# Performance work log

Measured on AMD Instinct MI355X. Metric: run time of the kernel, lower is better.

Reference implementation:

```python
import jax, jax.numpy as jnp
import numpy as np

D_MODEL = 1024
HIDDEN = 2048          # config.max_neurons
MOE_DIM = 64           # hardcoded moe_hidden_dim
N_EXPERTS = 8
TOP_K = 2
EXP_HIDDEN = HIDDEN // 2  # 1024
B, S = 4, 2048


def setup_inputs() -> dict:
    key = jax.random.key(0)
    ks = jax.random.split(key, 20)
    def w(k, shape, fan_in):
        return (jax.random.normal(k, shape, dtype=jnp.float32) / np.sqrt(fan_in)).astype(jnp.float32)
    return {
        "inputs_embeds": jax.random.normal(ks[0], (B, S, D_MODEL), dtype=jnp.float32),
        # GIFNeuron encoder (d_model -> hidden)
        "enc_w": w(ks[1], (D_MODEL, HIDDEN), D_MODEL),
        "enc_b": jnp.zeros((HIDDEN,), jnp.float32),
        # SpikeToContinuousBridge (hidden -> moe_dim)
        "s2c_w": w(ks[2], (HIDDEN, MOE_DIM), HIDDEN),
        "s2c_b": jnp.zeros((MOE_DIM,), jnp.float32),
        # LiquidMoERouter MLP (moe_dim -> 64 -> n_experts)
        "r_w1": w(ks[3], (MOE_DIM, 64), MOE_DIM),
        "r_b1": jnp.zeros((64,), jnp.float32),
        "r_w2": w(ks[4], (64, N_EXPERTS), 64),
        "r_b2": jnp.zeros((N_EXPERTS,), jnp.float32),
        # SNNExpert stacks (moe_dim -> exp_hidden -> moe_dim)
        "e_w1": w(ks[5], (N_EXPERTS, MOE_DIM, EXP_HIDDEN), MOE_DIM),
        "e_b1": jnp.zeros((N_EXPERTS, EXP_HIDDEN), jnp.float32),
        "e_w2": w(ks[6], (N_EXPERTS, EXP_HIDDEN, MOE_DIM), EXP_HIDDEN),
        "e_b2": jnp.zeros((N_EXPERTS, MOE_DIM), jnp.float32),
        # ContinuousToSpikeBridge (moe_dim -> hidden), poisson rates
        "c2s_w": w(ks[7], (MOE_DIM, HIDDEN), MOE_DIM),
        "c2s_b": jnp.zeros((HIDDEN,), jnp.float32),
        # GIFNeuron decoder (hidden -> d_model)
        "dec_w": w(ks[8], (HIDDEN, D_MODEL), HIDDEN),
        "dec_b": jnp.zeros((D_MODEL,), jnp.float32),
        # output LayerNorm
        "ln_g": jnp.ones((D_MODEL,), jnp.float32),
        "ln_b": jnp.zeros((D_MODEL,), jnp.float32),
    }


def reference(inputs_embeds, enc_w, enc_b, s2c_w, s2c_b, r_w1, r_b1, r_w2, r_b2,
              e_w1, e_b1, e_w2, e_b2, c2s_w, c2s_b, dec_w, dec_b, ln_g, ln_b):
    b, s, _ = inputs_embeds.shape
    # encoder GIF neuron: linear + sigmoid surrogate spikes -> [B,S,H]
    spikes = jax.nn.sigmoid(inputs_embeds @ enc_w + enc_b)
    # rate-decode (time axis of length 1 is identity) + projection -> [N, MOE_DIM]
    cont = spikes.reshape(b * s, -1) @ s2c_w + s2c_b
    # router: MLP -> softmax -> top-2 (renormalized)
    rh = jax.nn.relu(cont @ r_w1 + r_b1)
    probs = jax.nn.softmax(rh @ r_w2 + r_b2, axis=-1)          # [N, E]
    topw, topi = jax.lax.top_k(probs, TOP_K)                    # [N, K]
    topw = topw / jnp.sum(topw, axis=-1, keepdims=True)
    # combine weights per token per expert: sum_k w_k * [idx_k == e]
    comb = jnp.sum(jax.nn.one_hot(topi, N_EXPERTS, dtype=cont.dtype) * topw[..., None], axis=1)  # [N, E]
    # dense grouped expert compute (equivalent to masked gather/scatter loop)
    eh = jax.nn.relu(jnp.einsum('nd,edh->neh', cont, e_w1) + e_b1)   # [N, E, EXP_HIDDEN]
    eo = jnp.einsum('neh,ehd->ned', eh, e_w2) + e_b2                  # [N, E, MOE_DIM]
    moe_out = jnp.einsum('ned,ne->nd', eo, comb)                      # [N, MOE_DIM]
    # poisson-rate encode to spike space; mean over L identical rate steps == rates
    rates = jax.nn.sigmoid(moe_out @ c2s_w + c2s_b)                   # [N, H]
    x = rates.reshape(b, s, -1)
    # decoder GIF neuron + LayerNorm
    dec = jax.nn.sigmoid(x @ dec_w + dec_b)                           # [B, S, D]
    mu = jnp.mean(dec, axis=-1, keepdims=True)
    var = jnp.var(dec, axis=-1, keepdims=True)
    return (dec - mu) * jax.lax.rsqrt(var + 1e-5) * ln_g + ln_b
```

## Files before the change

kernel.cpp:

```cpp
#include <hip/hip_runtime.h>
#include <hip/hip_bf16.h>
#include <math.h>

typedef float  f32x4  __attribute__((ext_vector_type(4)));
typedef __bf16 bf16x8 __attribute__((ext_vector_type(8)));

__device__ __forceinline__ unsigned short f2bf(float f){
  union { float f; unsigned u; } v; v.f = f;
  unsigned u = v.u;
  return (unsigned short)((u + 0x7FFFu + ((u >> 16) & 1u)) >> 16);
}
__device__ __forceinline__ float bf2f(unsigned short h){
  union { unsigned u; float f; } v; v.u = ((unsigned)h) << 16;
  return v.f;
}
__device__ __forceinline__ void gload_lds16(const void* g, void* l){
  __builtin_amdgcn_global_load_lds((__attribute__((address_space(1))) void*)g,
                                   (__attribute__((address_space(3))) void*)l, 16, 0, 0);
}
__device__ __forceinline__ float sigmoidf_(float x){ return 1.f / (1.f + expf(-x)); }

__global__ __launch_bounds__(256)
void split_x_kernel(const float* __restrict__ X, unsigned short* __restrict__ A){
  for (int i = blockIdx.x*256 + threadIdx.x; i < 8192*1024; i += gridDim.x*256){
    int row = i >> 10, col = i & 1023;
    float x = X[i];
    unsigned short h = f2bf(x);
    unsigned short l = f2bf(x - bf2f(h));
    unsigned short* Ar = A + (size_t)row*3072 + col;
    Ar[0]    = h;
    Ar[1024] = l;
    Ar[2048] = h;
  }
}

__global__ __launch_bounds__(256)
void prep_tiles(const float* __restrict__ enc_w, const float* __restrict__ dec_w,
                const float* __restrict__ e_w1, const float* __restrict__ e_w2,
                const float* __restrict__ c2s_w,
                unsigned short* __restrict__ BtE, unsigned short* __restrict__ decT,
                unsigned short* __restrict__ W1T, unsigned short* __restrict__ W2T,
                unsigned short* __restrict__ c2sT)
{
  __shared__ unsigned tile[64*65];
  const int t = threadIdx.x;
  const int b = blockIdx.x;

  const float* src; long sbase; int sld, r0, c0;
  if (b < 512)        { src = enc_w; sbase = 0;                    sld = 2048; r0 = (b>>5)*64;       c0 = (b&31)*64; }
  else if (b < 1024)  { int q=b-512;  src = dec_w; sbase = 0;      sld = 1024; r0 = (q>>4)*64;       c0 = (q&15)*64; }
  else if (b < 1152)  { int q=b-1024; src = e_w1;  sbase = (long)(q>>4)*65536; sld = 1024; r0 = 0;   c0 = (q&15)*64; }
  else if (b < 1280)  { int q=b-1152; src = e_w2;  sbase = (long)(q>>4)*65536; sld = 64;   r0 = (q&15)*64; c0 = 0; }
  else                { int q=b-1280; src = c2s_w; sbase = 0;      sld = 2048; r0 = 0;              c0 = q*64; }

  #pragma unroll
  for (int it = 0; it < 4; ++it){
    int r  = it*16 + (t>>4);
    int c4 = (t&15)*4;
    float4 v = *(const float4*)&src[sbase + (long)(r0+r)*sld + c0 + c4];
    float vv[4] = {v.x, v.y, v.z, v.w};
    #pragma unroll
    for (int e = 0; e < 4; ++e){
      unsigned short h = f2bf(vv[e]);
      unsigned short l = f2bf(vv[e] - bf2f(h));
      tile[(c4+e)*65 + r] = (unsigned)h | ((unsigned)l << 16);
    }
  }
  __syncthreads();

  #pragma unroll
  for (int it = 0; it < 2; ++it){
    int c  = it*32 + (t>>3);
    int kc = (t&7)*8;
    unsigned short hi8[8], lo8[8];
    #pragma unroll
    for (int e = 0; e < 8; ++e){
      unsigned p = tile[c*65 + kc + e];
      hi8[e] = (unsigned short)(p & 0xFFFFu);
      lo8[e] = (unsigned short)(p >> 16);
    }
    if (b < 512){
      unsigned short* dst = BtE + (size_t)(c0 + c)*3072 + r0 + kc;
      *(uint4*)(dst)        = *(const uint4*)hi8;
      *(uint4*)(dst + 1024) = *(const uint4*)hi8;
      *(uint4*)(dst + 2048) = *(const uint4*)lo8;
    } else if (b < 1024){
      *(uint4*)(decT + (size_t)(c0 + c)*2048 + r0 + kc) = *(const uint4*)hi8;
    } else if (b < 1152){
      int e = (b-1024) >> 4;
      *(uint4*)(W1T + ((size_t)e<<16) + (size_t)(c0 + c)*64 + kc) = *(const uint4*)hi8;
    } else if (b < 1280){
      int e = (b-1152) >> 4;
      *(uint4*)(W2T + ((size_t)e<<16) + (size_t)(c0 + c)*1024 + r0 + kc) = *(const uint4*)hi8;
    } else {
      *(uint4*)(c2sT + (size_t)(c0 + c)*64 + kc) = *(const uint4*)hi8;
    }
  }
}

template<int SIG, int OBF>
__global__ __launch_bounds__(256)
void gemm_bt(const unsigned short* __restrict__ A, const unsigned short* __restrict__ Bt,
             const float* __restrict__ bias, void* __restrict__ C,
             int M, int N, int K)
{
  __shared__ alignas(16) unsigned short As[128*64];
  __shared__ alignas(16) unsigned short Bs[128*64];
  const int t = threadIdx.x;
  const int wid = t >> 6, lane = t & 63;
  const int nbn = N >> 7;
  const int q = gridDim.x >> 3;
  const int bid = (int)blockIdx.x;
  const int sb = (bid & 7) * q + (bid >> 3);
  const int bm = sb / nbn, bn = sb % nbn;
  const int wm = wid >> 1, wn = wid & 1;

  f32x4 acc[4][4];
  #pragma unroll
  for (int i=0;i<4;++i)
    #pragma unroll
    for (int j=0;j<4;++j) acc[i][j] = (f32x4){0.f,0.f,0.f,0.f};

  const size_t Kb = (size_t)K * 2;
  const char* Ab = (const char*)A  + (size_t)(bm*128) * Kb;
  const char* Bb = (const char*)Bt + (size_t)(bn*128) * Kb;

  for (int k0 = 0; k0 < K; k0 += 64){
    #pragma unroll
    for (int i = 0; i < 4; ++i){
      int L  = ((i*4 + wid) << 10) + (lane << 4);
      int r  = L >> 7;
      int cb = L & 127;
      int sb2 = cb ^ ((r & 7) << 4);
      gload_lds16(Ab + (size_t)r*Kb + (size_t)k0*2 + sb2, (char*)As + ((i*4+wid)<<10));
      gload_lds16(Bb + (size_t)r*Kb + (size_t)k0*2 + sb2, (char*)Bs + ((i*4+wid)<<10));
    }
    __syncthreads();
    #pragma unroll
    for (int ks = 0; ks < 64; ks += 32){
      bf16x8 af[4], bg[4];
      const int cb = ks*2 + ((lane >> 4) << 4);
      #pragma unroll
      for (int i = 0; i < 4; ++i){
        int ra = wm*64 + i*16 + (lane & 15);
        af[i] = *(const bf16x8*)((const char*)As + (ra<<7) + (cb ^ ((ra&7)<<4)));
        int rb = wn*64 + i*16 + (lane & 15);
        bg[i] = *(const bf16x8*)((const char*)Bs + (rb<<7) + (cb ^ ((rb&7)<<4)));
      }
      #pragma unroll
      for (int i = 0; i < 4; ++i)
        #pragma unroll
        for (int j = 0; j < 4; ++j)
          acc[i][j] = __builtin_amdgcn_mfma_f32_16x16x32_bf16(af[i], bg[j], acc[i][j], 0, 0, 0);
    }
    __syncthreads();
  }

  const int mrow0 = bm*128 + wm*64;
  const int ncol0 = bn*128 + wn*64;
  #pragma unroll
  for (int i = 0; i < 4; ++i){
    int row = mrow0 + i*16 + ((lane>>4)<<2);
    #pragma unroll
    for (int j = 0; j < 4; ++j){
      int col = ncol0 + j*16 + (lane & 15);
      float bv = bias[col];
      #pragma unroll
      for (int r = 0; r < 4; ++r){
        float v = acc[i][j][r] + bv;
        if (SIG) v = sigmoidf_(v);
        if (OBF) ((unsigned short*)C)[(size_t)(row + r)*N + col] = f2bf(v);
        else     ((float*)C)[(size_t)(row + r)*N + col] = v;
      }
    }
  }
}

__global__ __launch_bounds__(256)
void s2c_split(const float* __restrict__ spikes, const float* __restrict__ w,
               float* __restrict__ part)
{
  __shared__ float wS[4][64*64];
  const int t = threadIdx.x, wid = t >> 6, lane = t & 63;
  const int tg = blockIdx.x >> 2;
  const int ck = ((blockIdx.x & 3) << 2) | wid;
  const int tok = tg*64 + lane;
  const int k0 = ck * 128;

  float acc[64];
  #pragma unroll
  for (int j=0;j<64;++j) acc[j] = 0.f;

  const float* srow = spikes + (size_t)tok*2048 + k0;
  float* wsp = wS[wid];

  for (int half = 0; half < 2; ++half){
    const float* gsrc = w + (size_t)(k0 + half*64)*64;
    #pragma unroll
    for (int it = 0; it < 16; ++it){
      int idx = (it*64 + lane)*4;
      *(float4*)&wsp[idx] = *(const float4*)&gsrc[idx];
    }
    #pragma unroll 2
    for (int kq = 0; kq < 16; ++kq){
      float4 s4 = *(const float4*)&srow[half*64 + kq*4];
      const float sv[4] = {s4.x, s4.y, s4.z, s4.w};
      #pragma unroll
      for (int ki = 0; ki < 4; ++ki){
        const float* wrow = &wsp[(kq*4+ki)*64];
        #pragma unroll
        for (int j4 = 0; j4 < 16; ++j4){
          float4 wv = *(const float4*)&wrow[j4*4];
          acc[j4*4+0] += sv[ki] * wv.x;
          acc[j4*4+1] += sv[ki] * wv.y;
          acc[j4*4+2] += sv[ki] * wv.z;
          acc[j4*4+3] += sv[ki] * wv.w;
        }
      }
    }
  }
  float* po = part + ((size_t)ck*8192 + tok)*64;
  #pragma unroll
  for (int j4 = 0; j4 < 16; ++j4){
    float4 o; o.x = acc[j4*4+0]; o.y = acc[j4*4+1]; o.z = acc[j4*4+2]; o.w = acc[j4*4+3];
    *(float4*)&po[j4*4] = o;
  }
}

__global__ __launch_bounds__(256)
void s2c_reduce(const float* __restrict__ part, const float* __restrict__ bias,
                float* __restrict__ cont, unsigned short* __restrict__ contbf)
{
  int i4 = blockIdx.x*256 + threadIdx.x;
  int base = i4 * 4;
  float4 a = {0.f,0.f,0.f,0.f};
  #pragma unroll
  for (int c = 0; c < 16; ++c){
    float4 p = *(const float4*)&part[(size_t)c*524288 + base];
    a.x += p.x; a.y += p.y; a.z += p.z; a.w += p.w;
  }
  int j0 = base & 63;
  float4 b = *(const float4*)&bias[j0];
  a.x += b.x; a.y += b.y; a.z += b.z; a.w += b.w;
  *(float4*)&cont[base] = a;
  unsigned short h0 = f2bf(a.x), h1 = f2bf(a.y), h2 = f2bf(a.z), h3 = f2bf(a.w);
  unsigned u0 = ((unsigned)h1 << 16) | h0;
  unsigned u1 = ((unsigned)h3 << 16) | h2;
  uint2 u; u.x = u0; u.y = u1;
  *(uint2*)&contbf[base] = u;
}

__global__ __launch_bounds__(256)
void router_kernel(const float* __restrict__ cont, const float* __restrict__ w1,
                   const float* __restrict__ b1, const float* __restrict__ w2,
                   const float* __restrict__ b2, float* __restrict__ comb)
{
  __shared__ float w1s[64*64];
  __shared__ float w2s[64*8];
  __shared__ float b1s[64], b2s[8];
  __shared__ float rhs[4][64];
  const int t = threadIdx.x;
  for (int i = t; i < 64*64; i += 256) w1s[i] = w1[i];
  for (int i = t; i < 64*8;  i += 256) w2s[i] = w2[i];
  if (t < 64) b1s[t] = b1[t];
  if (t < 8)  b2s[t] = b2[t];
  __syncthreads();
  const int wid = t >> 6, lane = t & 63;
  const int gw = blockIdx.x*4 + wid, nw = gridDim.x*4;
  for (int n = gw; n < 8192; n += nw){
    float cv = cont[(size_t)n*64 + lane];
    float rh = b1s[lane];
    #pragma unroll
    for (int d = 0; d < 64; ++d){
      float cd = __shfl(cv, d);
      rh += cd * w1s[d*64 + lane];
    }
    rh = fmaxf(rh, 0.f);
    rhs[wid][lane] = rh;
    __syncthreads();
    float lg[8];
    #pragma unroll
    for (int e = 0; e < 8; ++e) lg[e] = b2s[e];
    for (int jj = 0; jj < 64; ++jj){
      float r = rhs[wid][jj];
      #pragma unroll
      for (int e = 0; e < 8; ++e) lg[e] += r * w2s[jj*8 + e];
    }
    int i1 = 0; float m1 = lg[0];
    #pragma unroll
    for (int e = 1; e < 8; ++e) if (lg[e] > m1){ m1 = lg[e]; i1 = e; }
    int i2 = -1; float m2 = -3.4e38f;
    #pragma unroll
    for (int e = 0; e < 8; ++e) if (e != i1 && lg[e] > m2){ m2 = lg[e]; i2 = e; }
    float e2 = expf(m2 - m1);
    float wA = 1.f / (1.f + e2);
    float wB = e2 / (1.f + e2);
    if (lane < 8) comb[(size_t)n*8 + lane] = (lane == i1) ? wA : ((lane == i2) ? wB : 0.f);
    __syncthreads();
  }
}

__global__ __launch_bounds__(256)
void expert_kernel(const unsigned short* __restrict__ contbf, const float* __restrict__ comb,
                   const unsigned short* __restrict__ W1T, const unsigned short* __restrict__ W2T,
                   const float* __restrict__ e_b1, const float* __restrict__ e_b2,
                   float* __restrict__ part)
{
  __shared__ alignas(16) unsigned short contS[64*64];
  __shared__ alignas(16) unsigned short w1S[64*64];
  __shared__ alignas(16) unsigned short w2S[64*64];
  __shared__ alignas(16) unsigned short ehS[64*64];
  __shared__ float combS[64*8];
  const int t = threadIdx.x, wid = t >> 6, lane = t & 63;
  const int tb = blockIdx.x >> 2, z = blockIdx.x & 3;
  const int tok0 = tb * 64;

  #pragma unroll
  for (int it = 0; it < 2; ++it){
    int li = (it*256 + t)*8;
    int r = li >> 6, c = li & 63;
    uint4 v = *(const uint4*)(contbf + (size_t)(tok0 + r)*64 + c);
    *(uint4*)((char*)contS + (r<<7) + ((c*2) ^ ((r&7)<<4))) = v;
  }
  for (int i = t; i < 512; i += 256) combS[i] = comb[(size_t)tok0*8 + i];

  f32x4 macc[4];
  #pragma unroll
  for (int j=0;j<4;++j) macc[j] = (f32x4){0.f,0.f,0.f,0.f};

  for (int ei = 0; ei < 2; ++ei){
    const int e = z*2 + ei;
    f32x4 eo[4];
    #pragma unroll
    for (int j=0;j<4;++j) eo[j] = (f32x4){0.f,0.f,0.f,0.f};

    for (int hc = 0; hc < 16; ++hc){
      const int h0 = hc*64;
      __syncthreads();
      #pragma unroll
      for (int it = 0; it < 2; ++it){
        int li = (it*256 + t)*8;
        int r = li >> 6, c = li & 63;
        uint4 v1 = *(const uint4*)(W1T + ((size_t)e<<16) + (size_t)(h0+r)*64 + c);
        *(uint4*)((char*)w1S + (r<<7) + ((c*2) ^ ((r&7)<<4))) = v1;
        uint4 v2 = *(const uint4*)(W2T + ((size_t)e<<16) + (size_t)r*1024 + h0 + c);
        *(uint4*)((char*)w2S + (r<<7) + ((c*2) ^ ((r&7)<<4))) = v2;
      }
      __syncthreads();
      f32x4 eh[4];
      #pragma unroll
      for (int j=0;j<4;++j) eh[j] = (f32x4){0.f,0.f,0.f,0.f};
      #pragma unroll
      for (int ks = 0; ks < 64; ks += 32){
        const int cb = ks*2 + ((lane>>4)<<4);
        int ra = wid*16 + (lane & 15);
        bf16x8 av = *(const bf16x8*)((const char*)contS + (ra<<7) + (cb ^ ((ra&7)<<4)));
        #pragma unroll
        for (int j=0;j<4;++j){
          int rb = j*16 + (lane & 15);
          bf16x8 bv = *(const bf16x8*)((const char*)w1S + (rb<<7) + (cb ^ ((rb&7)<<4)));
          eh[j] = __builtin_amdgcn_mfma_f32_16x16x32_bf16(av, bv, eh[j], 0, 0, 0);
        }
      }
      #pragma unroll
      for (int j=0;j<4;++j){
        int colh = j*16 + (lane & 15);
        float b1v = e_b1[e*1024 + h0 + colh];
        #pragma unroll
        for (int r=0;r<4;++r){
          int rowt = wid*16 + ((lane>>4)<<2) + r;
          float v = fmaxf(eh[j][r] + b1v, 0.f);
          *(unsigned short*)((char*)ehS + (rowt<<7) + ((colh*2) ^ ((rowt&7)<<4))) = f2bf(v);
        }
      }
      __syncthreads();
      #pragma unroll
      for (int ks = 0; ks < 64; ks += 32){
        const int cb = ks*2 + ((lane>>4)<<4);
        int ra = wid*16 + (lane & 15);
        bf16x8 av = *(const bf16x8*)((const char*)ehS + (ra<<7) + (cb ^ ((ra&7)<<4)));
        #pragma unroll
        for (int j=0;j<4;++j){
          int rb = j*16 + (lane & 15);
          bf16x8 bv = *(const bf16x8*)((const char*)w2S + (rb<<7) + (cb ^ ((rb&7)<<4)));
          eo[j] = __builtin_amdgcn_mfma_f32_16x16x32_bf16(av, bv, eo[j], 0, 0, 0);
        }
      }
    }
    #pragma unroll
    for (int j=0;j<4;++j){
      int col = j*16 + (lane & 15);
      float b2v = e_b2[e*64 + col];
      #pragma unroll
      for (int r=0;r<4;++r){
        int rowt = wid*16 + ((lane>>4)<<2) + r;
        float w = combS[rowt*8 + e];
        macc[j][r] += w * (eo[j][r] + b2v);
      }
    }
  }
  #pragma unroll
  for (int j=0;j<4;++j){
    int col = j*16 + (lane & 15);
    #pragma unroll
    for (int r=0;r<4;++r){
      int rowt = wid*16 + ((lane>>4)<<2) + r;
      part[((size_t)z*8192 + tok0 + rowt)*64 + col] = macc[j][r];
    }
  }
}

__global__ __launch_bounds__(256)
void reduce_moe(const float* __restrict__ part, unsigned short* __restrict__ moebf){
  int i = blockIdx.x*256 + threadIdx.x;
  if (i < 8192*64){
    float v = part[i] + part[i + 524288] + part[i + 2*524288] + part[i + 3*524288];
    moebf[i] = f2bf(v);
  }
}

__global__ __launch_bounds__(256)
void ln_kernel(const float* __restrict__ dec, const float* __restrict__ g,
               const float* __restrict__ b, float* __restrict__ out){
  const int wid = threadIdx.x >> 6, lane = threadIdx.x & 63;
  const int row = blockIdx.x*4 + wid;
  const float4* x4 = (const float4*)(dec + (size_t)row*1024);
  float4 v[4]; float s = 0.f, s2 = 0.f;
  #pragma unroll
  for (int i=0;i<4;++i){
    v[i] = x4[lane + i*64];
    s  += (v[i].x + v[i].y) + (v[i].z + v[i].w);
    s2 += (v[i].x*v[i].x + v[i].y*v[i].y) + (v[i].z*v[i].z + v[i].w*v[i].w);
  }
  #pragma unroll
  for (int o = 32; o > 0; o >>= 1){ s += __shfl_xor(s, o); s2 += __shfl_xor(s2, o); }
  float mu  = s * (1.f/1024.f);
  float var = s2 * (1.f/1024.f) - mu*mu;
  float inv = rsqrtf(var + 1e-5f);
  float4* o4 = (float4*)(out + (size_t)row*1024);
  #pragma unroll
  for (int i=0;i<4;++i){
    int c0 = (lane + i*64)*4;
    float4 r;
    r.x = (v[i].x - mu)*inv*g[c0+0] + b[c0+0];
    r.y = (v[i].y - mu)*inv*g[c0+1] + b[c0+1];
    r.z = (v[i].z - mu)*inv*g[c0+2] + b[c0+2];
    r.w = (v[i].w - mu)*inv*g[c0+3] + b[c0+3];
    o4[lane + i*64] = r;
  }
}

extern "C" void kernel_launch(void* const* d_in, const int* in_sizes, int n_in,
                              void* d_out, int out_size, void* d_ws, size_t ws_size,
                              hipStream_t stream)
{
  (void)in_sizes; (void)n_in; (void)out_size; (void)ws_size;
  const float* X     = (const float*)d_in[0];
  const float* enc_w = (const float*)d_in[1];
  const float* enc_b = (const float*)d_in[2];
  const float* s2c_w = (const float*)d_in[3];
  const float* s2c_b = (const float*)d_in[4];
  const float* r_w1  = (const float*)d_in[5];
  const float* r_b1  = (const float*)d_in[6];
  const float* r_w2  = (const float*)d_in[7];
  const float* r_b2  = (const float*)d_in[8];
  const float* e_w1  = (const float*)d_in[9];
  const float* e_b1  = (const float*)d_in[10];
  const float* e_w2  = (const float*)d_in[11];
  const float* e_b2  = (const float*)d_in[12];
  const float* c2s_w = (const float*)d_in[13];
  const float* c2s_b = (const float*)d_in[14];
  const float* dec_w = (const float*)d_in[15];
  const float* dec_b = (const float*)d_in[16];
  const float* ln_g  = (const float*)d_in[17];
  const float* ln_b  = (const float*)d_in[18];

  char* ws = (char*)d_ws;
  size_t off = 0;
  auto alloc = [&](size_t bytes){ void* p = ws + off; off += (bytes + 255) & ~(size_t)255; return p; };
  unsigned short* Axs    = (unsigned short*)alloc(8192ULL*3072*2);
  unsigned short* BtE    = (unsigned short*)alloc(2048ULL*3072*2);
  float*          spikes = (float*)alloc(8192ULL*2048*4);
  float*          cont   = (float*)alloc(8192ULL*64*4);
  unsigned short* contbf = (unsigned short*)alloc(8192ULL*64*2);
  float*          comb   = (float*)alloc(8192ULL*8*4);
  unsigned short* W1T    = (unsigned short*)alloc(8ULL*1024*64*2);
  unsigned short* W2T    = (unsigned short*)alloc(8ULL*64*1024*2);
  unsigned short* moebf  = (unsigned short*)alloc(8192ULL*64*2);
  unsigned short* c2sT   = (unsigned short*)alloc(2048ULL*64*2);
  unsigned short* decT   = (unsigned short*)alloc(1024ULL*2048*2);
  float*          part   = (float*)Axs;
  unsigned short* rates  = Axs;
  float*          decf   = spikes;
  float*          outp   = (float*)d_out;

  split_x_kernel<<<dim3(4096), dim3(256), 0, stream>>>(X, Axs);
  prep_tiles<<<dim3(1312), dim3(256), 0, stream>>>(enc_w, dec_w, e_w1, e_w2, c2s_w,
                                                   BtE, decT, W1T, W2T, c2sT);
  gemm_bt<1,0><<<dim3(64*16), dim3(256), 0, stream>>>(Axs, BtE, enc_b, (void*)spikes, 8192, 2048, 3072);
  s2c_split<<<dim3(512), dim3(256), 0, stream>>>(spikes, s2c_w, part);
  s2c_reduce<<<dim3(512), dim3(256), 0, stream>>>(part, s2c_b, cont, contbf);
  router_kernel<<<dim3(512), dim3(256), 0, stream>>>(cont, r_w1, r_b1, r_w2, r_b2, comb);
  expert_kernel<<<dim3(512), dim3(256), 0, stream>>>(contbf, comb, W1T, W2T, e_b1, e_b2, part);
  reduce_moe<<<dim3(2048), dim3(256), 0, stream>>>(part, moebf);
  gemm_bt<1,1><<<dim3(64*16), dim3(256), 0, stream>>>(moebf, c2sT, c2s_b, (void*)rates, 8192, 2048, 64);
  gemm_bt<1,0><<<dim3(64*8), dim3(256), 0, stream>>>(rates, decT, dec_b, (void*)decf, 8192, 1024, 2048);
  ln_kernel<<<dim3(2048), dim3(256), 0, stream>>>(decf, ln_g, ln_b, outp);
}
```

Before: 498.0 us.

## Replace encoder GEMM with 256x256-tile, 8-wave, 4-stage pipelined kernel

Adds a new bf16 MFMA GEMM kernel (gemm8) for the encoder projection. It uses 256x256 output tiles, 512 threads per block, a 4-deep LDS ring buffer filled by direct global-to-LDS loads, XOR-swizzled LDS addressing and setprio around the MFMA bursts. The aim is more reuse per byte loaded and better overlap of loads with compute than the previous 128x128 kernel. The cost is 128 KB of LDS per block, so one block per CU, and only 256 blocks for 256 CUs, with a single wave of work.

```diff
diff --git a/kernel.cpp b/kernel.cpp
--- a/kernel.cpp
+++ b/kernel.cpp
@@ -94,6 +94,93 @@
       *(uint4*)(W2T + ((size_t)e<<16) + (size_t)(c0 + c)*1024 + r0 + kc) = *(const uint4*)hi8;
     } else {
       *(uint4*)(c2sT + (size_t)(c0 + c)*64 + kc) = *(const uint4*)hi8;
+    }
+  }
+}
+
+__global__ __launch_bounds__(512)
+void gemm8(const unsigned short* __restrict__ A, const unsigned short* __restrict__ Bt,
+           const float* __restrict__ bias, float* __restrict__ C,
+           int M, int N, int K)
+{
+  __shared__ alignas(16) char AsB[4][16384];
+  __shared__ alignas(16) char BsB[4][16384];
+  const int t = threadIdx.x, w = t >> 6, lane = t & 63;
+  const int nbn = N >> 8;
+  const int qq = gridDim.x >> 3, bid = (int)blockIdx.x;
+  const int sbk = (bid & 7) * qq + (bid >> 3);
+  const int bm = sbk / nbn, bn = sbk % nbn;
+  const int wm = w >> 2, wn = w & 3;
+
+  f32x4 acc[8][4];
+  #pragma unroll
+  for (int m=0;m<8;++m)
+    #pragma unroll
+    for (int n=0;n<4;++n) acc[m][n] = (f32x4){0.f,0.f,0.f,0.f};
+
+  const size_t Kb = (size_t)K * 2;
+  const char* Ab = (const char*)A  + (size_t)(bm*256) * Kb;
+  const char* Bb = (const char*)Bt + (size_t)(bn*256) * Kb;
+  const int nt = K >> 5;
+
+  auto STAGE = [&](int kt){
+    char* Ad = AsB[kt & 3]; char* Bd = BsB[kt & 3];
+    #pragma unroll
+    for (int i = 0; i < 2; ++i){
+      int chunk = w*2 + i;
+      int row   = chunk*16 + (lane >> 2);
+      int sw    = (((lane & 3) ^ ((row >> 1) & 3)) << 4);
+      gload_lds16(Ab + (size_t)row*Kb + (size_t)kt*64 + sw, Ad + chunk*1024);
+      gload_lds16(Bb + (size_t)row*Kb + (size_t)kt*64 + sw, Bd + chunk*1024);
+    }
+  };
+
+  STAGE(0); STAGE(1); STAGE(2);
+  asm volatile("s_waitcnt vmcnt(8)" ::: "memory");
+  __builtin_amdgcn_s_barrier();
+
+  for (int t0 = 0; t0 < nt; ++t0){
+    const char* Ar = AsB[t0 & 3];
+    const char* Br = BsB[t0 & 3];
+    bf16x8 af[8], bg[4];
+    #pragma unroll
+    for (int m = 0; m < 8; ++m){
+      int ra = wm*128 + m*16 + (lane & 15);
+      af[m] = *(const bf16x8*)(Ar + ra*64 + ((((lane>>4) ^ ((ra>>1)&3))) << 4));
+    }
+    #pragma unroll
+    for (int n = 0; n < 4; ++n){
+      int rb = wn*64 + n*16 + (lane & 15);
+      bg[n] = *(const bf16x8*)(Br + rb*64 + ((((lane>>4) ^ ((rb>>1)&3))) << 4));
+    }
+    if (t0 + 3 < nt) STAGE(t0 + 3);
+    __builtin_amdgcn_s_setprio(1);
+    #pragma unroll
+    for (int m = 0; m < 8; ++m)
+      #pragma unroll
+      for (int n = 0; n < 4; ++n)
+        acc[m][n] = __builtin_amdgcn_mfma_f32_16x16x32_bf16(af[m], bg[n], acc[m][n], 0, 0, 0);
+    __builtin_amdgcn_s_setprio(0);
+    if (t0 + 3 < nt)      asm volatile("s_waitcnt vmcnt(8)" ::: "memory");
+    else if (t0 + 2 < nt) asm volatile("s_waitcnt vmcnt(4)" ::: "memory");
+    else                  asm volatile("s_waitcnt vmcnt(0)" ::: "memory");
+    __builtin_amdgcn_s_barrier();
+  }
+
+  const int mrow0 = bm*256 + wm*128;
+  const int ncol0 = bn*256 + wn*64;
+  #pragma unroll
+  for (int m = 0; m < 8; ++m){
+    int row = mrow0 + m*16 + ((lane>>4)<<2);
+    #pragma unroll
+    for (int n = 0; n < 4; ++n){
+      int col = ncol0 + n*16 + (lane & 15);
+      float bv = bias[col];
+      #pragma unroll
+      for (int r = 0; r < 4; ++r){
+        float v = sigmoidf_(acc[m][n][r] + bv);
+        C[(size_t)(row + r)*N + col] = v;
+      }
     }
   }
 }
@@ -497,7 +584,7 @@
   split_x_kernel<<<dim3(4096), dim3(256), 0, stream>>>(X, Axs);
   prep_tiles<<<dim3(1312), dim3(256), 0, stream>>>(enc_w, dec_w, e_w1, e_w2, c2s_w,
                                                    BtE, decT, W1T, W2T, c2sT);
-  gemm_bt<1,0><<<dim3(64*16), dim3(256), 0, stream>>>(Axs, BtE, enc_b, (void*)spikes, 8192, 2048, 3072);
+  gemm8<<<dim3(256), dim3(512), 0, stream>>>(Axs, BtE, enc_b, spikes, 8192, 2048, 3072);
   s2c_split<<<dim3(512), dim3(256), 0, stream>>>(spikes, s2c_w, part);
   s2c_reduce<<<dim3(512), dim3(256), 0, stream>>>(part, s2c_b, cont, contbf);
   router_kernel<<<dim3(512), dim3(256), 0, stream>>>(cont, r_w1, r_b1, r_w2, r_b2, comb);
```

Result: no change. 488.8 us (-1.8%).
